# Kernel optimization log

Measured on AMD Instinct MI355X. Metric: run time of the kernel, lower is better.

The kernel has to match this reference:

```python
import jax, jax.numpy as jnp
import numpy as np

B, S, D, H = 2, 2048, 2048, 16
HD = D // H  # head_dim = 128
ROPE_BASE = 10000.0


def _rope_interleaved(x, cos, sin):
    # x: [B, S, H, HD]; cos/sin: [S, HD//2]
    xe = x[..., 0::2]
    xo = x[..., 1::2]
    c = cos[None, :, None, :]
    s = sin[None, :, None, :]
    oe = xe * c - xo * s
    oo = xe * s + xo * c
    # re-interleave pairs back to last dim
    return jnp.stack([oe, oo], axis=-1).reshape(x.shape)


def setup_inputs() -> dict:
    key = jax.random.key(0)
    k0, k1, k2, k3 = jax.random.split(key, 4)
    scale = D ** -0.5
    x = jax.random.normal(k0, (B, S, D), dtype=jnp.float32)
    wqk = jax.random.normal(k1, (2 * D, D), dtype=jnp.float32) * scale
    wv = jax.random.normal(k2, (D, D), dtype=jnp.float32) * scale
    wo = jax.random.normal(k3, (D, D), dtype=jnp.float32) * scale
    return {"x": x, "wqk": wqk, "wv": wv, "wo": wo}


def reference(x, wqk, wv, wo):
    b, s, d = x.shape
    # fused QK projection -> [B, S, 2, H, HD]
    xqk = (x @ wqk.T).reshape(b, s, 2, H, HD)
    xq = xqk[:, :, 0]
    xk = xqk[:, :, 1]
    xv = (x @ wv.T).reshape(b, s, H, HD)

    # interleaved rotary embedding (seqlen_offset=0, no-cache path)
    inv_freq = 1.0 / (ROPE_BASE ** (jnp.arange(0, HD, 2, dtype=jnp.float32) / HD))
    freqs = jnp.arange(s, dtype=jnp.float32)[:, None] * inv_freq[None, :]  # [S, HD//2]
    cos, sin = jnp.cos(freqs), jnp.sin(freqs)
    xq = _rope_interleaved(xq, cos, sin)
    xk = _rope_interleaved(xk, cos, sin)

    # causal scaled-dot-product attention
    scores = jnp.einsum("bqhd,bkhd->bhqk", xq, xk) * (HD ** -0.5)
    causal = jnp.tril(jnp.ones((s, s), dtype=bool))
    scores = jnp.where(causal[None, None], scores, jnp.finfo(scores.dtype).min)
    probs = jax.nn.softmax(scores, axis=-1)
    out = jnp.einsum("bhqk,bkhd->bqhd", probs, xv).reshape(b, s, d)
    return out @ wo.T
```

## Files before the change

### kernel.cpp

```cpp
#include <hip/hip_runtime.h>
#include <hip/hip_bf16.h>

#define NB 2
#define SEQ 2048
#define DMODEL 2048
#define NH 16
#define HD 128
#define QSCALE (0.08838834764831845f * 1.44269504088896f)
#define THRL2 11.5f

using bf16x8 = __attribute__((ext_vector_type(8))) __bf16;
using f32x4  = __attribute__((ext_vector_type(4))) float;

#define MFMA16 __builtin_amdgcn_mfma_f32_16x16x32_bf16

typedef __attribute__((address_space(1))) const void* gptr_t;
typedef __attribute__((address_space(3))) void* lptr_t;

__device__ inline void gload_lds16(const unsigned short* g, unsigned short* l) {
    __builtin_amdgcn_global_load_lds((gptr_t)g, (lptr_t)l, 16, 0, 0);
}

__device__ inline unsigned short f2b(float f) {
    unsigned u = __builtin_bit_cast(unsigned, f);
    u += 0x7FFF + ((u >> 16) & 1);
    return (unsigned short)(u >> 16);
}
__device__ inline float b2f(unsigned short h) {
    return __builtin_bit_cast(float, (unsigned)h << 16);
}
__device__ inline float fexp2(float x) {
    float r;
    asm("v_exp_f32 %0, %1" : "=v"(r) : "v"(x));
    return r;
}
__device__ inline unsigned cvtpk(float a, float b) {
    unsigned r;
    asm("v_cvt_pk_bf16_f32 %0, %1, %2" : "=v"(r) : "v"(a), "v"(b));
    return r;
}

__global__ void cast_all(const float* __restrict__ x, const float* __restrict__ wqk,
                         const float* __restrict__ wv, const float* __restrict__ wo,
                         unsigned short* __restrict__ xb, unsigned short* __restrict__ wb,
                         float2* __restrict__ tab) {
    int idx = blockIdx.x * 256 + threadIdx.x;
    if (idx < 6291456) {
        const float* src; unsigned short* dst; int off;
        if (idx < 2097152)      { src = x;   dst = xb;             off = 0; }
        else if (idx < 4194304) { src = wqk; dst = wb;             off = 2097152; }
        else if (idx < 5242880) { src = wv;  dst = wb + 8388608;   off = 4194304; }
        else                    { src = wo;  dst = wb + 12582912;  off = 5242880; }
        int i = (idx - off) * 4;
        float4 v = *reinterpret_cast<const float4*>(src + i);
        ushort4 o;
        o.x = f2b(v.x); o.y = f2b(v.y); o.z = f2b(v.z); o.w = f2b(v.w);
        *reinterpret_cast<ushort4*>(dst + i) = o;
    } else {
        int k = idx - 6291456;
        int i = k & 63;
        int s = k >> 6;
        float inv = exp2f(-13.287712379549449f * (float)i * (1.0f / 64.0f));
        float ang = (float)s * inv;
        float sn, cs;
        sincosf(ang, &sn, &cs);
        tab[k] = make_float2(cs, sn);
    }
}

template<int MODE>
__global__ __launch_bounds__(512) void gemm8p(const unsigned short* __restrict__ A,
                                              const unsigned short* __restrict__ Bw,
                                              void* __restrict__ Cout,
                                              unsigned short* __restrict__ qb,
                                              unsigned short* __restrict__ kbp,
                                              unsigned short* __restrict__ vt,
                                              const float2* __restrict__ tab,
                                              int M, int N, int K) {
    __shared__ __align__(16) char lds[98304];
    int tid = threadIdx.x;
    int lane = tid & 63;
    int wid = tid >> 6;
    int wm = wid >> 2, wn = wid & 3;
    int row0 = blockIdx.y * 128;
    int col0 = blockIdx.x * 256;
    int lr = lane & 15, g = lane >> 4;

    const unsigned short* srcA[2];
    const unsigned short* srcB[4];
#pragma unroll
    for (int i = 0; i < 2; i++) {
        int chunk = i * 512 + tid;
        int ksub = chunk >> 9;
        int cw = chunk & 511;
        int row = cw >> 2, c = cw & 3;
        int cs = c ^ ((row >> 1) & 3);
        srcA[i] = A + (size_t)(row0 + row) * K + ksub * 32 + cs * 8;
    }
#pragma unroll
    for (int i = 0; i < 4; i++) {
        int chunk = i * 512 + tid;
        int ksub = chunk >> 10;
        int cw = chunk & 1023;
        int row = cw >> 2, c = cw & 3;
        int cs = c ^ ((row >> 1) & 3);
        srcB[i] = Bw + (size_t)(col0 + row) * K + ksub * 32 + cs * 8;
    }

    int offA[4][2], offB[4][2];
#pragma unroll
    for (int i = 0; i < 4; i++) {
        int row = wm * 64 + i * 16 + lr;
#pragma unroll
        for (int ks = 0; ks < 2; ks++)
            offA[i][ks] = ks * 8192 + row * 64 + ((g ^ ((row >> 1) & 3)) * 16);
    }
#pragma unroll
    for (int j = 0; j < 4; j++) {
        int row = wn * 64 + j * 16 + lr;
#pragma unroll
        for (int ks = 0; ks < 2; ks++)
            offB[j][ks] = ks * 16384 + row * 64 + ((g ^ ((row >> 1) & 3)) * 16);
    }

    f32x4 acc[4][4] = {};
    int NT = K >> 6;

#define STAGE8(t) {                                                                   \
        int kb_ = (t) * 64;                                                           \
        int bs_ = ((t) & 1) * 49152;                                                  \
        _Pragma("unroll")                                                             \
        for (int i_ = 0; i_ < 2; i_++)                                                \
            gload_lds16(srcA[i_] + kb_,                                               \
                (unsigned short*)(lds + bs_ + (i_ * 512 + (tid & ~63)) * 16));        \
        _Pragma("unroll")                                                             \
        for (int i_ = 0; i_ < 4; i_++)                                                \
            gload_lds16(srcB[i_] + kb_,                                               \
                (unsigned short*)(lds + bs_ + 16384 + (i_ * 512 + (tid & ~63)) * 16)); \
    }

    STAGE8(0);
    for (int t = 0; t < NT; ++t) {
        if (t + 1 < NT) {
            STAGE8(t + 1);
            asm volatile("s_waitcnt vmcnt(6)" ::: "memory");
        } else {
            asm volatile("s_waitcnt vmcnt(0)" ::: "memory");
        }
        __builtin_amdgcn_s_barrier();
        __builtin_amdgcn_sched_barrier(0);

        const char* ab = lds + (t & 1) * 49152;
        const char* bb = ab + 16384;

        bf16x8 b[4][2], a[2][2];
#pragma unroll
        for (int j = 0; j < 4; j++)
#pragma unroll
            for (int ks = 0; ks < 2; ks++)
                b[j][ks] = *reinterpret_cast<const bf16x8*>(bb + offB[j][ks]);
#pragma unroll
        for (int i = 0; i < 2; i++)
#pragma unroll
            for (int ks = 0; ks < 2; ks++)
                a[i][ks] = *reinterpret_cast<const bf16x8*>(ab + offA[i][ks]);
        asm volatile("s_waitcnt lgkmcnt(0)" ::: "memory");
        __builtin_amdgcn_sched_barrier(0);
        __builtin_amdgcn_s_setprio(1);
#pragma unroll
        for (int ks = 0; ks < 2; ks++)
#pragma unroll
            for (int i = 0; i < 2; i++)
#pragma unroll
                for (int j = 0; j < 4; j++)
                    acc[i][j] = MFMA16(a[i][ks], b[j][ks], acc[i][j], 0, 0, 0);
        __builtin_amdgcn_s_setprio(0);

        bf16x8 a2[2][2];
#pragma unroll
        for (int i = 0; i < 2; i++)
#pragma unroll
            for (int ks = 0; ks < 2; ks++)
                a2[i][ks] = *reinterpret_cast<const bf16x8*>(ab + offA[2 + i][ks]);
        asm volatile("s_waitcnt lgkmcnt(0)" ::: "memory");
        __builtin_amdgcn_sched_barrier(0);
        __builtin_amdgcn_s_barrier();
        __builtin_amdgcn_sched_barrier(0);
        __builtin_amdgcn_s_setprio(1);
#pragma unroll
        for (int ks = 0; ks < 2; ks++)
#pragma unroll
            for (int i = 0; i < 2; i++)
#pragma unroll
                for (int j = 0; j < 4; j++)
                    acc[2 + i][j] = MFMA16(a2[i][ks], b[j][ks], acc[2 + i][j], 0, 0, 0);
        __builtin_amdgcn_s_setprio(0);
    }
#undef STAGE8

    int orow = g * 4;
    if (MODE == 0) {
#pragma unroll
        for (int i = 0; i < 4; i++) {
#pragma unroll
            for (int j = 0; j < 4; j++) {
                int r0 = row0 + wm * 64 + i * 16 + orow;
                int c  = col0 + wn * 64 + j * 16 + lr;
#pragma unroll
                for (int r = 0; r < 4; r++)
                    ((float*)Cout)[(size_t)(r0 + r) * N + c] = acc[i][j][r];
            }
        }
    } else {
        int bx = blockIdx.x;
        if (bx < 16) {
            const bool isQ = (bx < 8);
            unsigned short* dst = isQ ? qb : kbp;
#pragma unroll
            for (int i = 0; i < 4; i++) {
#pragma unroll
                for (int j = 0; j < 4; j++) {
                    int c = col0 + wn * 64 + j * 16 + lr;
                    int cc = c & 2047;
                    int h = cc >> 7, d = cc & 127, i2 = d >> 1;
                    int odd = lr & 1;
#pragma unroll
                    for (int r = 0; r < 4; r++) {
                        int trow = row0 + wm * 64 + i * 16 + orow + r;
                        int s = trow & (SEQ - 1), bb2 = trow >> 11;
                        float v = acc[i][j][r];
                        float pv = __shfl_xor(v, 1);
                        float2 cssn = tab[s * 64 + i2];
                        float out = odd ? (pv * cssn.y + v * cssn.x)
                                        : (v * cssn.x - pv * cssn.y);
                        if (isQ) out *= QSCALE;
                        dst[((size_t)((bb2 * NH + h) * SEQ + s)) * HD + d] = f2b(out);
                    }
                }
            }
        } else {
#pragma unroll
            for (int i = 0; i < 4; i++) {
#pragma unroll
                for (int j = 0; j < 4; j++) {
                    int cc = col0 + wn * 64 + j * 16 + lr - 4096;
                    int h = cc >> 7, d = cc & 127;
                    int trow0 = row0 + wm * 64 + i * 16 + orow;
                    int s0 = trow0 & (SEQ - 1), bb2 = trow0 >> 11;
                    int bh = bb2 * NH + h;
                    ushort4 o4;
                    o4.x = f2b(acc[i][j][0]);
                    o4.y = f2b(acc[i][j][1]);
                    o4.z = f2b(acc[i][j][2]);
                    o4.w = f2b(acc[i][j][3]);
                    *reinterpret_cast<ushort4*>(vt + ((size_t)bh * HD + d) * SEQ + s0) = o4;
                }
            }
        }
    }
}

__global__ __launch_bounds__(64, 2) void attn10(const unsigned short* __restrict__ Q,
                                                const unsigned short* __restrict__ Kb,
                                                const unsigned short* __restrict__ Vt,
                                                unsigned short* __restrict__ O) {
    __shared__ __align__(16) char lds[20480];

    int lane = threadIdx.x;
    int bid = blockIdx.x;
    int qt = 63 - (bid >> 5);
    int bh = bid & 31;
    int q0 = qt * 32;
    int ktiles = (qt >> 1) + 1;
    int lr = lane & 15;
    int g  = lane >> 4;
    int g4 = g * 4;
    int lk = g * 8;

    const unsigned short* Qp = Q  + (size_t)bh * SEQ * HD;
    const unsigned short* Kp = Kb + (size_t)bh * SEQ * HD;
    const unsigned short* Vp = Vt + (size_t)bh * HD * SEQ;
    char* pl = lds + 16384;
    int b = bh >> 4;
    int h = bh & 15;

    int srcoff[16];
#pragma unroll
    for (int i2 = 0; i2 < 16; ++i2) {
        int r = i2 * 4 + g;
        srcoff[i2] = r * HD + ((lr ^ (r & 7)) * 8);
    }

#define STAGEK64(kvbase)                                                            \
    {                                                                               \
        const unsigned short* kbase = Kp + (size_t)(kvbase) * HD;                   \
        _Pragma("unroll")                                                           \
        for (int i2 = 0; i2 < 16; ++i2)                                             \
            gload_lds16(kbase + srcoff[i2],                                         \
                        (unsigned short*)(lds + i2 * 1024));                        \
    }

    bf16x8 qf[2][4];
#pragma unroll
    for (int f = 0; f < 2; f++)
#pragma unroll
        for (int kb = 0; kb < 4; kb++)
            qf[f][kb] = *reinterpret_cast<const bf16x8*>(Qp + (size_t)(q0 + f * 16 + lr) * HD + kb * 32 + lk);

    f32x4 oacc[2][8] = {};
    float m[2] = { -1e30f, -1e30f }, l[2] = { 0.0f, 0.0f };
    int qrow[2] = { q0 + lr, q0 + 16 + lr };

    STAGEK64(0);

    for (int t = 0; t < ktiles; ++t) {
        int kv0 = t * 64;
        asm volatile("s_waitcnt vmcnt(0)" ::: "memory");
        __builtin_amdgcn_sched_barrier(0);

        f32x4 s[2][4] = {};
#pragma unroll
        for (int kb = 0; kb < 4; kb++) {
#pragma unroll
            for (int jj = 0; jj < 4; jj++) {
                int row = jj * 16 + lr;
                int cin = ((kb * 4 + g) ^ (row & 7));
                bf16x8 kf = *reinterpret_cast<const bf16x8*>(lds + row * 256 + cin * 16);
                s[0][jj] = MFMA16(kf, qf[0][kb], s[0][jj], 0, 0, 0);
                s[1][jj] = MFMA16(kf, qf[1][kb], s[1][jj], 0, 0, 0);
            }
        }

        bf16x8 vf[8][2];
#pragma unroll
        for (int db = 0; db < 8; db++)
#pragma unroll
            for (int ks = 0; ks < 2; ks++)
                vf[db][ks] = *reinterpret_cast<const bf16x8*>(Vp + (size_t)(db * 16 + lr) * SEQ + kv0 + ks * 32 + lk);

#pragma unroll
        for (int f = 0; f < 2; f++) {
            int q = qrow[f];
            bool full = (kv0 + 63 <= q0 + f * 16);
            float mx = -1e30f;
            if (full) {
#pragma unroll
                for (int jj = 0; jj < 4; jj++)
#pragma unroll
                    for (int r = 0; r < 4; r++)
                        mx = fmaxf(mx, s[f][jj][r]);
            } else {
#pragma unroll
                for (int jj = 0; jj < 4; jj++)
#pragma unroll
                    for (int r = 0; r < 4; r++) {
                        int kv = kv0 + jj * 16 + g4 + r;
                        float v = (kv <= q) ? s[f][jj][r] : -1e30f;
                        s[f][jj][r] = v;
                        mx = fmaxf(mx, v);
                    }
            }
            mx = fmaxf(mx, __shfl_xor(mx, 16));
            mx = fmaxf(mx, __shfl_xor(mx, 32));

            if (!__all(mx <= m[f] + THRL2)) {
                float mn = fmaxf(m[f], mx);
                float sc = fexp2(m[f] - mn);
                m[f] = mn;
                l[f] *= sc;
#pragma unroll
                for (int db = 0; db < 8; db++)
#pragma unroll
                    for (int r = 0; r < 4; r++)
                        oacc[f][db][r] *= sc;
            }

            int row = f * 16 + lr;
            int rb = row * 128;
            int sw = (row & 7) << 4;
            float rs = 0.0f;
#pragma unroll
            for (int jj = 0; jj < 4; jj++)
#pragma unroll
                for (int hh = 0; hh < 2; hh++) {
                    float p0 = fexp2(s[f][jj][2 * hh]     - m[f]);
                    float p1 = fexp2(s[f][jj][2 * hh + 1] - m[f]);
                    rs += p0 + p1;
                    unsigned pk = cvtpk(p0, p1);
                    int colb = jj * 32 + g * 8 + 4 * hh;
                    *reinterpret_cast<unsigned*>(pl + rb + (colb ^ sw)) = pk;
                }
            rs += __shfl_xor(rs, 16);
            rs += __shfl_xor(rs, 32);
            l[f] += rs;
        }

        asm volatile("s_waitcnt lgkmcnt(0)" ::: "memory");
        __builtin_amdgcn_sched_barrier(0);

        if (t + 1 < ktiles) STAGEK64(kv0 + 64);

        bf16x8 pb[2][2];
#pragma unroll
        for (int f = 0; f < 2; f++)
#pragma unroll
            for (int ks = 0; ks < 2; ks++) {
                int row = f * 16 + lr;
                int off = row * 128 + ((ks * 64 + g * 16) ^ ((row & 7) << 4));
                pb[f][ks] = *reinterpret_cast<const bf16x8*>(pl + off);
            }
#pragma unroll
        for (int db = 0; db < 8; db++)
#pragma unroll
            for (int ks = 0; ks < 2; ks++) {
                oacc[0][db] = MFMA16(vf[db][ks], pb[0][ks], oacc[0][db], 0, 0, 0);
                oacc[1][db] = MFMA16(vf[db][ks], pb[1][ks], oacc[1][db], 0, 0, 0);
            }
    }

#pragma unroll
    for (int f = 0; f < 2; f++) {
        float inv = 1.0f / l[f];
        int q = q0 + f * 16 + lr;
        unsigned short* op = O + ((size_t)(b * SEQ + q)) * DMODEL + h * HD;
#pragma unroll
        for (int db = 0; db < 8; db++) {
            ushort4 o4;
            o4.x = f2b(oacc[f][db][0] * inv);
            o4.y = f2b(oacc[f][db][1] * inv);
            o4.z = f2b(oacc[f][db][2] * inv);
            o4.w = f2b(oacc[f][db][3] * inv);
            *reinterpret_cast<ushort4*>(op + db * 16 + g4) = o4;
        }
    }
#undef STAGEK64
}

extern "C" void kernel_launch(void* const* d_in, const int* in_sizes, int n_in,
                              void* d_out, int out_size, void* d_ws, size_t ws_size,
                              hipStream_t stream) {
    const float* x   = (const float*)d_in[0];
    const float* wqk = (const float*)d_in[1];
    const float* wv  = (const float*)d_in[2];
    const float* wo  = (const float*)d_in[3];

    unsigned short* xb  = (unsigned short*)d_ws;
    unsigned short* wb  = xb  + (size_t)8388608;
    unsigned short* qb  = wb  + (size_t)16777216;
    unsigned short* kb  = qb  + (size_t)8388608;
    unsigned short* vt  = kb  + (size_t)8388608;
    unsigned short* ao  = vt  + (size_t)8388608;
    float2* tab = (float2*)(ao + (size_t)8388608);

    cast_all<<<25088, 256, 0, stream>>>(x, wqk, wv, wo, xb, wb, tab);

    gemm8p<2><<<dim3(24, 32), 512, 0, stream>>>(xb, wb, nullptr, qb, kb, vt, tab, 4096, 6144, 2048);

    attn10<<<2048, 64, 0, stream>>>(qb, kb, vt, ao);

    gemm8p<0><<<dim3(8, 32), 512, 0, stream>>>(ao, wb + 12582912, d_out, nullptr, nullptr, nullptr, nullptr, 4096, 2048, 2048);
}
```

Measured before the change: 270.8 us.

## Use 128x128-tile 256-thread GEMM for fused QKV projection with RoPE epilogue

Adds a new gemm128 kernel for the QKV projection, using 128x128 output tiles, 4 waves and double-buffered 64-wide K stages in 64KB LDS, in place of the 128x256 8-wave tile. It launches 1536 blocks instead of 768, which spreads the work more evenly across the MI355X's CUs and may allow more blocks per CU because of the smaller LDS footprint. The RoPE, Q-scale and V-transpose epilogue moves into this kernel, and gemm8p is simplified to the plain fp32 output projection. The trade-off is less operand reuse per tile, so more global and LDS traffic per FLOP.

```diff
diff --git a/kernel.cpp b/kernel.cpp
--- a/kernel.cpp
+++ b/kernel.cpp
@@ -68,14 +68,176 @@
     }
 }
 
-template<int MODE>
+__global__ __launch_bounds__(256) void gemm128(const unsigned short* __restrict__ A,
+                                               const unsigned short* __restrict__ Bw,
+                                               unsigned short* __restrict__ qb,
+                                               unsigned short* __restrict__ kbp,
+                                               unsigned short* __restrict__ vt,
+                                               const float2* __restrict__ tab,
+                                               int M, int N, int K) {
+    __shared__ __align__(16) char lds[65536];
+    int tid = threadIdx.x;
+    int lane = tid & 63;
+    int wid = tid >> 6;
+    int wm = wid >> 1, wn = wid & 1;
+    int row0 = blockIdx.y * 128;
+    int col0 = blockIdx.x * 128;
+    int lr = lane & 15, g = lane >> 4;
+
+    const unsigned short* srcA[4];
+    const unsigned short* srcB[4];
+#pragma unroll
+    for (int i = 0; i < 4; i++) {
+        int chunk = i * 256 + tid;
+        int ksub = chunk >> 9;
+        int cw = chunk & 511;
+        int row = cw >> 2, c = cw & 3;
+        int cs = c ^ ((row >> 1) & 3);
+        srcA[i] = A  + (size_t)(row0 + row) * K + ksub * 32 + cs * 8;
+        srcB[i] = Bw + (size_t)(col0 + row) * K + ksub * 32 + cs * 8;
+    }
+
+    int offA[4][2], offB[4][2];
+#pragma unroll
+    for (int i = 0; i < 4; i++) {
+        int row = wm * 64 + i * 16 + lr;
+#pragma unroll
+        for (int ks = 0; ks < 2; ks++)
+            offA[i][ks] = ks * 8192 + row * 64 + ((g ^ ((row >> 1) & 3)) * 16);
+    }
+#pragma unroll
+    for (int j = 0; j < 4; j++) {
+        int row = wn * 64 + j * 16 + lr;
+#pragma unroll
+        for (int ks = 0; ks < 2; ks++)
+            offB[j][ks] = 16384 + ks * 8192 + row * 64 + ((g ^ ((row >> 1) & 3)) * 16);
+    }
+
+    f32x4 acc[4][4] = {};
+    int NT = K >> 6;
+
+#define STAGE1x(t) {                                                                  \
+        int kb_ = (t) * 64;                                                           \
+        int bs_ = ((t) & 1) * 32768;                                                  \
+        _Pragma("unroll")                                                             \
+        for (int i_ = 0; i_ < 4; i_++)                                                \
+            gload_lds16(srcA[i_] + kb_,                                               \
+                (unsigned short*)(lds + bs_ + (i_ * 256 + (tid & ~63)) * 16));        \
+        _Pragma("unroll")                                                             \
+        for (int i_ = 0; i_ < 4; i_++)                                                \
+            gload_lds16(srcB[i_] + kb_,                                               \
+                (unsigned short*)(lds + bs_ + 16384 + (i_ * 256 + (tid & ~63)) * 16)); \
+    }
+
+    STAGE1x(0);
+    for (int t = 0; t < NT; ++t) {
+        if (t + 1 < NT) {
+            STAGE1x(t + 1);
+            asm volatile("s_waitcnt vmcnt(8)" ::: "memory");
+        } else {
+            asm volatile("s_waitcnt vmcnt(0)" ::: "memory");
+        }
+        __builtin_amdgcn_s_barrier();
+        __builtin_amdgcn_sched_barrier(0);
+
+        const char* ab = lds + (t & 1) * 32768;
+
+        bf16x8 b[4][2], a[2][2];
+#pragma unroll
+        for (int j = 0; j < 4; j++)
+#pragma unroll
+            for (int ks = 0; ks < 2; ks++)
+                b[j][ks] = *reinterpret_cast<const bf16x8*>(ab + offB[j][ks]);
+#pragma unroll
+        for (int i = 0; i < 2; i++)
+#pragma unroll
+            for (int ks = 0; ks < 2; ks++)
+                a[i][ks] = *reinterpret_cast<const bf16x8*>(ab + offA[i][ks]);
+        asm volatile("s_waitcnt lgkmcnt(0)" ::: "memory");
+        __builtin_amdgcn_sched_barrier(0);
+        __builtin_amdgcn_s_setprio(1);
+#pragma unroll
+        for (int ks = 0; ks < 2; ks++)
+#pragma unroll
+            for (int i = 0; i < 2; i++)
+#pragma unroll
+                for (int j = 0; j < 4; j++)
+                    acc[i][j] = MFMA16(a[i][ks], b[j][ks], acc[i][j], 0, 0, 0);
+        __builtin_amdgcn_s_setprio(0);
+
+        bf16x8 a2[2][2];
+#pragma unroll
+        for (int i = 0; i < 2; i++)
+#pragma unroll
+            for (int ks = 0; ks < 2; ks++)
+                a2[i][ks] = *reinterpret_cast<const bf16x8*>(ab + offA[2 + i][ks]);
+        asm volatile("s_waitcnt lgkmcnt(0)" ::: "memory");
+        __builtin_amdgcn_sched_barrier(0);
+        __builtin_amdgcn_s_barrier();
+        __builtin_amdgcn_sched_barrier(0);
+        __builtin_amdgcn_s_setprio(1);
+#pragma unroll
+        for (int ks = 0; ks < 2; ks++)
+#pragma unroll
+            for (int i = 0; i < 2; i++)
+#pragma unroll
+                for (int j = 0; j < 4; j++)
+                    acc[2 + i][j] = MFMA16(a2[i][ks], b[j][ks], acc[2 + i][j], 0, 0, 0);
+        __builtin_amdgcn_s_setprio(0);
+    }
+#undef STAGE1x
+
+    int orow = g * 4;
+    int bx = blockIdx.x;
+    if (bx < 32) {
+        const bool isQ = (bx < 16);
+        unsigned short* dst = isQ ? qb : kbp;
+#pragma unroll
+        for (int i = 0; i < 4; i++) {
+#pragma unroll
+            for (int j = 0; j < 4; j++) {
+                int c = col0 + wn * 64 + j * 16 + lr;
+                int cc = c & 2047;
+                int h = cc >> 7, d = cc & 127, i2 = d >> 1;
+                int odd = lr & 1;
+#pragma unroll
+                for (int r = 0; r < 4; r++) {
+                    int trow = row0 + wm * 64 + i * 16 + orow + r;
+                    int s = trow & (SEQ - 1), bb2 = trow >> 11;
+                    float v = acc[i][j][r];
+                    float pv = __shfl_xor(v, 1);
+                    float2 cssn = tab[s * 64 + i2];
+                    float out = odd ? (pv * cssn.y + v * cssn.x)
+                                    : (v * cssn.x - pv * cssn.y);
+                    if (isQ) out *= QSCALE;
+                    dst[((size_t)((bb2 * NH + h) * SEQ + s)) * HD + d] = f2b(out);
+                }
+            }
+        }
+    } else {
+#pragma unroll
+        for (int i = 0; i < 4; i++) {
+#pragma unroll
+            for (int j = 0; j < 4; j++) {
+                int cc = (col0 + wn * 64 + j * 16 + lr) & 2047;
+                int h = cc >> 7, d = cc & 127;
+                int trow0 = row0 + wm * 64 + i * 16 + orow;
+                int s0 = trow0 & (SEQ - 1), bb2 = trow0 >> 11;
+                int bh = bb2 * NH + h;
+                ushort4 o4;
+                o4.x = f2b(acc[i][j][0]);
+                o4.y = f2b(acc[i][j][1]);
+                o4.z = f2b(acc[i][j][2]);
+                o4.w = f2b(acc[i][j][3]);
+                *reinterpret_cast<ushort4*>(vt + ((size_t)bh * HD + d) * SEQ + s0) = o4;
+            }
+        }
+    }
+}
+
 __global__ __launch_bounds__(512) void gemm8p(const unsigned short* __restrict__ A,
                                               const unsigned short* __restrict__ Bw,
-                                              void* __restrict__ Cout,
-                                              unsigned short* __restrict__ qb,
-                                              unsigned short* __restrict__ kbp,
-                                              unsigned short* __restrict__ vt,
-                                              const float2* __restrict__ tab,
+                                              float* __restrict__ Cout,
                                               int M, int N, int K) {
     __shared__ __align__(16) char lds[98304];
     int tid = threadIdx.x;
@@ -199,63 +361,15 @@
 #undef STAGE8
 
     int orow = g * 4;
-    if (MODE == 0) {
-#pragma unroll
-        for (int i = 0; i < 4; i++) {
-#pragma unroll
-            for (int j = 0; j < 4; j++) {
-                int r0 = row0 + wm * 64 + i * 16 + orow;
-                int c  = col0 + wn * 64 + j * 16 + lr;
-#pragma unroll
-                for (int r = 0; r < 4; r++)
-                    ((float*)Cout)[(size_t)(r0 + r) * N + c] = acc[i][j][r];
-            }
-        }
-    } else {
-        int bx = blockIdx.x;
-        if (bx < 16) {
-            const bool isQ = (bx < 8);
-            unsigned short* dst = isQ ? qb : kbp;
-#pragma unroll
-            for (int i = 0; i < 4; i++) {
-#pragma unroll
-                for (int j = 0; j < 4; j++) {
-                    int c = col0 + wn * 64 + j * 16 + lr;
-                    int cc = c & 2047;
-                    int h = cc >> 7, d = cc & 127, i2 = d >> 1;
-                    int odd = lr & 1;
-#pragma unroll
-                    for (int r = 0; r < 4; r++) {
-                        int trow = row0 + wm * 64 + i * 16 + orow + r;
-                        int s = trow & (SEQ - 1), bb2 = trow >> 11;
-                        float v = acc[i][j][r];
-                        float pv = __shfl_xor(v, 1);
-                        float2 cssn = tab[s * 64 + i2];
-                        float out = odd ? (pv * cssn.y + v * cssn.x)
-                                        : (v * cssn.x - pv * cssn.y);
-                        if (isQ) out *= QSCALE;
-                        dst[((size_t)((bb2 * NH + h) * SEQ + s)) * HD + d] = f2b(out);
-                    }
-                }
-            }
-        } else {
-#pragma unroll
-            for (int i = 0; i < 4; i++) {
-#pragma unroll
-                for (int j = 0; j < 4; j++) {
-                    int cc = col0 + wn * 64 + j * 16 + lr - 4096;
-                    int h = cc >> 7, d = cc & 127;
-                    int trow0 = row0 + wm * 64 + i * 16 + orow;
-                    int s0 = trow0 & (SEQ - 1), bb2 = trow0 >> 11;
-                    int bh = bb2 * NH + h;
-                    ushort4 o4;
-                    o4.x = f2b(acc[i][j][0]);
-                    o4.y = f2b(acc[i][j][1]);
-                    o4.z = f2b(acc[i][j][2]);
-                    o4.w = f2b(acc[i][j][3]);
-                    *reinterpret_cast<ushort4*>(vt + ((size_t)bh * HD + d) * SEQ + s0) = o4;
-                }
-            }
+#pragma unroll
+    for (int i = 0; i < 4; i++) {
+#pragma unroll
+        for (int j = 0; j < 4; j++) {
+            int r0 = row0 + wm * 64 + i * 16 + orow;
+            int c  = col0 + wn * 64 + j * 16 + lr;
+#pragma unroll
+            for (int r = 0; r < 4; r++)
+                Cout[(size_t)(r0 + r) * N + c] = acc[i][j][r];
         }
     }
 }
@@ -454,9 +568,9 @@
 
     cast_all<<<25088, 256, 0, stream>>>(x, wqk, wv, wo, xb, wb, tab);
 
-    gemm8p<2><<<dim3(24, 32), 512, 0, stream>>>(xb, wb, nullptr, qb, kb, vt, tab, 4096, 6144, 2048);
+    gemm128<<<dim3(48, 32), 256, 0, stream>>>(xb, wb, qb, kb, vt, tab, 4096, 6144, 2048);
 
     attn10<<<2048, 64, 0, stream>>>(qb, kb, vt, ao);
 
-    gemm8p<0><<<dim3(8, 32), 512, 0, stream>>>(ao, wb + 12582912, d_out, nullptr, nullptr, nullptr, nullptr, 4096, 2048, 2048);
-}
+    gemm8p<<<dim3(8, 32), 512, 0, stream>>>(ao, wb + 12582912, (float*)d_out, 4096, 2048, 2048);
+}
```

After: 273.2 us. No clear change (+0.9%).
